# Kernel optimization log

Measured on AMD Instinct MI355X. Metric: run time of the kernel, lower is better.

The kernel has to match this reference:

```python
import jax, jax.numpy as jnp
import numpy as np

N, D, HID, ATT, B, NC = 131072, 1024, 256, 128, 64, 2
EPS = 1e-5

def _ln(h, g, b):
    mu = jnp.mean(h, axis=-1, keepdims=True)
    var = jnp.mean((h - mu) ** 2, axis=-1, keepdims=True)
    return (h - mu) * jax.lax.rsqrt(var + EPS) * g + b

def _gelu(x):
    return jax.nn.gelu(x, approximate=False)  # torch nn.GELU default (erf)

def setup_inputs() -> dict:
    key = jax.random.key(0)
    ks = jax.random.split(key, 16)
    def w(k, shape, fan_in):
        return (jax.random.normal(k, shape, jnp.float32) / np.sqrt(fan_in)).astype(jnp.float32)
    # sorted, every bag non-empty (~equal sizes)
    segment_ids = ((jnp.arange(N) * B) // N).astype(jnp.int32)
    return {
        "x": jax.random.normal(ks[0], (N, D), jnp.float32),
        "segment_ids": segment_ids,
        "W1": w(ks[1], (D, HID), D), "b1": jnp.zeros((HID,), jnp.float32),
        "g1": jnp.ones((HID,), jnp.float32), "be1": jnp.zeros((HID,), jnp.float32),
        "W2": w(ks[2], (HID, HID), HID), "b2": jnp.zeros((HID,), jnp.float32),
        "g2": jnp.ones((HID,), jnp.float32), "be2": jnp.zeros((HID,), jnp.float32),
        "Wv": w(ks[3], (HID, ATT), HID), "bv": jnp.zeros((ATT,), jnp.float32),
        "Wu": w(ks[4], (HID, ATT), HID), "bu": jnp.zeros((ATT,), jnp.float32),
        "Ww": w(ks[5], (ATT, 1), ATT), "bw": jnp.zeros((1,), jnp.float32),
        "Wc1": w(ks[6], (HID, HID // 2), HID), "bc1": jnp.zeros((HID // 2,), jnp.float32),
        "Wc2": w(ks[7], (HID // 2, NC), HID // 2), "bc2": jnp.zeros((NC,), jnp.float32),
    }

def reference(x, segment_ids, W1, b1, g1, be1, W2, b2, g2, be2,
              Wv, bv, Wu, bu, Ww, bw, Wc1, bc1, Wc2, bc2):
    # encoder (dropout = identity at inference)
    h = _gelu(_ln(x @ W1 + b1, g1, be1))          # [N, HID]
    h = _gelu(_ln(h @ W2 + b2, g2, be2))          # [N, HID]
    # gated attention logits
    a = (jnp.tanh(h @ Wv + bv) * jax.nn.sigmoid(h @ Wu + bu)) @ Ww + bw  # [N, 1]
    a = a[:, 0]                                    # [N]
    # per-bag (segment) softmax
    m = jax.ops.segment_max(a, segment_ids, num_segments=B)             # [B]
    e = jnp.exp(a - m[segment_ids])
    s = jax.ops.segment_sum(e, segment_ids, num_segments=B)             # [B]
    attn = e / s[segment_ids]                                           # [N]
    # attention-weighted bag pooling
    z = jax.ops.segment_sum(attn[:, None] * h, segment_ids, num_segments=B)  # [B, HID]
    # classifier
    logits = _gelu(z @ Wc1 + bc1) @ Wc2 + bc2       # [B, NC]
    return logits
```

## Files before the change

### kernel.cpp

```cpp
#include <hip/hip_runtime.h>
#include <math.h>

#define N_TOK  131072
#define DIM    1024
#define HIDN   256
#define ATTN   128
#define NSEG   64
#define SEGLEN 2048
#define NCLS   2
#define EPSLN  1e-5f

typedef __attribute__((ext_vector_type(8))) short  short8;
typedef __attribute__((ext_vector_type(4))) float  f32x4;

__device__ __forceinline__ unsigned short f2bf(float f) {
    unsigned int u = __float_as_uint(f);
    u += 0x7fffu + ((u >> 16) & 1u);
    return (unsigned short)(u >> 16);
}
__device__ __forceinline__ float bf2f(unsigned short h) {
    return __uint_as_float(((unsigned int)h) << 16);
}
__device__ __forceinline__ float gelu_exact(float x) {
    return 0.5f * x * (1.0f + erff(x * 0.70710678118654752f));
}

__global__ __launch_bounds__(256) void transpose_cvt(const float* __restrict__ in,
                                                     unsigned short* __restrict__ out,
                                                     int R, int C) {
    __shared__ float t[32][33];
    const int bx = blockIdx.x * 32;
    const int by = blockIdx.y * 32;
    const int x = threadIdx.x, y = threadIdx.y;
#pragma unroll
    for (int i = 0; i < 32; i += 8) {
        int r = by + y + i, c = bx + x;
        if (r < R && c < C) t[y + i][x] = in[(size_t)r * C + c];
    }
    __syncthreads();
#pragma unroll
    for (int i = 0; i < 32; i += 8) {
        int c = bx + y + i, r = by + x;
        if (c < C && r < R) out[(size_t)c * R + r] = f2bf(t[x][y + i]);
    }
}

__global__ void build_bvu(const float* __restrict__ bv, const float* __restrict__ bu,
                          float* __restrict__ bvu) {
    int t = threadIdx.x;
    bvu[t] = (t < 128) ? bv[t] : bu[t - 128];
}

template <int K, bool AF32>
__global__ __launch_bounds__(256) void gemm_bf16(const void* __restrict__ Aptr,
                                                 const unsigned short* __restrict__ Wt,
                                                 const float* __restrict__ bias,
                                                 float* __restrict__ C) {
    __shared__ unsigned short As[64][40];
    __shared__ unsigned short Ws[256][40];
    const int tid  = threadIdx.x;
    const int wave = tid >> 6, lane = tid & 63;
    const int lr = lane & 15, lq = lane >> 4;
    const int srow = tid >> 2, skq = (tid & 3) * 8;
    const size_t row0 = (size_t)blockIdx.x * 64;

    f32x4 acc[4][4];
#pragma unroll
    for (int i = 0; i < 4; i++)
#pragma unroll
        for (int j = 0; j < 4; j++) acc[i][j] = (f32x4)0.0f;

    for (int k0 = 0; k0 < K; k0 += 32) {
        short8 aw;
        if constexpr (AF32) {
            const float* A = (const float*)Aptr;
            const float* p = &A[(row0 + srow) * K + k0 + skq];
            float4 v0 = *(const float4*)p;
            float4 v1 = *(const float4*)(p + 4);
            aw[0] = (short)f2bf(v0.x); aw[1] = (short)f2bf(v0.y);
            aw[2] = (short)f2bf(v0.z); aw[3] = (short)f2bf(v0.w);
            aw[4] = (short)f2bf(v1.x); aw[5] = (short)f2bf(v1.y);
            aw[6] = (short)f2bf(v1.z); aw[7] = (short)f2bf(v1.w);
        } else {
            const unsigned short* A = (const unsigned short*)Aptr;
            aw = *(const short8*)&A[(row0 + srow) * K + k0 + skq];
        }
        short8 ww[4];
#pragma unroll
        for (int c = 0; c < 4; c++)
            ww[c] = *(const short8*)&Wt[(size_t)(srow + 64 * c) * K + k0 + skq];

        __syncthreads();
        *(short8*)&As[srow][skq] = aw;
#pragma unroll
        for (int c = 0; c < 4; c++)
            *(short8*)&Ws[srow + 64 * c][skq] = ww[c];
        __syncthreads();

        short8 a[4], b[4];
#pragma unroll
        for (int i = 0; i < 4; i++) a[i] = *(const short8*)&As[16 * i + lr][lq * 8];
#pragma unroll
        for (int j = 0; j < 4; j++) b[j] = *(const short8*)&Ws[64 * wave + 16 * j + lr][lq * 8];
#pragma unroll
        for (int i = 0; i < 4; i++)
#pragma unroll
            for (int j = 0; j < 4; j++)
                acc[i][j] = __builtin_amdgcn_mfma_f32_16x16x32_bf16(a[i], b[j], acc[i][j], 0, 0, 0);
    }

    float bj[4];
#pragma unroll
    for (int j = 0; j < 4; j++) bj[j] = bias[wave * 64 + 16 * j + lr];
#pragma unroll
    for (int i = 0; i < 4; i++)
#pragma unroll
        for (int j = 0; j < 4; j++)
#pragma unroll
            for (int r = 0; r < 4; r++)
                C[(row0 + 16 * i + lq * 4 + r) * 256 + wave * 64 + 16 * j + lr] = acc[i][j][r] + bj[j];
}

__global__ __launch_bounds__(256) void ln_gelu_cvt(const float* __restrict__ Cin,
                                                   const float* __restrict__ g,
                                                   const float* __restrict__ be,
                                                   unsigned short* __restrict__ Hout) {
    const int row  = blockIdx.x * 4 + (threadIdx.x >> 6);
    const int lane = threadIdx.x & 63;
    float4 v = *(const float4*)&Cin[(size_t)row * HIDN + lane * 4];
    float s  = v.x + v.y + v.z + v.w;
    float sq = v.x * v.x + v.y * v.y + v.z * v.z + v.w * v.w;
#pragma unroll
    for (int o = 32; o > 0; o >>= 1) { s += __shfl_down(s, o); sq += __shfl_down(sq, o); }
    s  = __shfl(s, 0);
    sq = __shfl(sq, 0);
    const float mu  = s * (1.0f / HIDN);
    const float var = sq * (1.0f / HIDN) - mu * mu;
    const float r   = rsqrtf(var + EPSLN);
    float4 gg = *(const float4*)&g[lane * 4];
    float4 bb = *(const float4*)&be[lane * 4];
    ushort4 o4;
    o4.x = f2bf(gelu_exact((v.x - mu) * r * gg.x + bb.x));
    o4.y = f2bf(gelu_exact((v.y - mu) * r * gg.y + bb.y));
    o4.z = f2bf(gelu_exact((v.z - mu) * r * gg.z + bb.z));
    o4.w = f2bf(gelu_exact((v.w - mu) * r * gg.w + bb.w));
    *(ushort4*)&Hout[(size_t)row * HIDN + lane * 4] = o4;
}

__global__ __launch_bounds__(256) void score_act(const float* __restrict__ VU,
                                                 const float* __restrict__ Ww,
                                                 const float* __restrict__ bw,
                                                 float* __restrict__ Aout) {
    const int row  = blockIdx.x * 4 + (threadIdx.x >> 6);
    const int lane = threadIdx.x & 63;
    const float* p = VU + (size_t)row * 256;
    float2 v = *(const float2*)&p[2 * lane];
    float2 u = *(const float2*)&p[128 + 2 * lane];
    float2 w = *(const float2*)&Ww[2 * lane];
    float val = tanhf(v.x) * (1.0f / (1.0f + expf(-u.x))) * w.x
              + tanhf(v.y) * (1.0f / (1.0f + expf(-u.y))) * w.y;
#pragma unroll
    for (int o = 32; o > 0; o >>= 1) val += __shfl_down(val, o);
    if (lane == 0) Aout[row] = val + bw[0];
}

__global__ __launch_bounds__(256) void seg_softmax(float* __restrict__ A) {
    __shared__ float red[256];
    const int seg = blockIdx.x, tid = threadIdx.x;
    float* a = A + (size_t)seg * SEGLEN;
    float m = -1e30f;
#pragma unroll
    for (int c = 0; c < 8; c++) m = fmaxf(m, a[tid + 256 * c]);
    red[tid] = m; __syncthreads();
    for (int s = 128; s > 0; s >>= 1) {
        if (tid < s) red[tid] = fmaxf(red[tid], red[tid + s]);
        __syncthreads();
    }
    m = red[0]; __syncthreads();
    float e[8]; float sum = 0.0f;
#pragma unroll
    for (int c = 0; c < 8; c++) { e[c] = expf(a[tid + 256 * c] - m); sum += e[c]; }
    red[tid] = sum; __syncthreads();
    for (int s = 128; s > 0; s >>= 1) {
        if (tid < s) red[tid] += red[tid + s];
        __syncthreads();
    }
    const float inv = 1.0f / red[0];
#pragma unroll
    for (int c = 0; c < 8; c++) a[tid + 256 * c] = e[c] * inv;
}

__global__ __launch_bounds__(256) void pool_partial(const float* __restrict__ Attn,
                                                    const unsigned short* __restrict__ H,
                                                    float* __restrict__ Zp) {
    __shared__ float aw[256];
    const int tid = threadIdx.x;
    const size_t rbase = (size_t)blockIdx.x * 256;
    aw[tid] = Attn[rbase + tid];
    __syncthreads();
    const unsigned short* h = H + rbase * 256 + tid;
    float acc = 0.0f;
    for (int r = 0; r < 256; r++) acc += aw[r] * bf2f(h[(size_t)r * 256]);
    Zp[rbase + tid] = acc;
}

__global__ __launch_bounds__(256) void head_kernel(const float* __restrict__ Zp,
                                                   const float* __restrict__ Wc1,
                                                   const float* __restrict__ bc1,
                                                   const float* __restrict__ Wc2,
                                                   const float* __restrict__ bc2,
                                                   float* __restrict__ Out) {
    __shared__ float zs[256];
    __shared__ float hs[128];
    __shared__ float red[4];
    const int seg = blockIdx.x, tid = threadIdx.x;
    float z = 0.0f;
#pragma unroll
    for (int c = 0; c < 8; c++) z += Zp[((size_t)seg * 8 + c) * 256 + tid];
    zs[tid] = z;
    __syncthreads();
    if (tid < 128) {
        float acc = bc1[tid];
        for (int k = 0; k < 256; k++) acc += zs[k] * Wc1[k * 128 + tid];
        hs[tid] = gelu_exact(acc);
    }
    __syncthreads();
    const int cls = tid >> 7, j = tid & 127;
    float val = hs[j] * Wc2[j * 2 + cls];
#pragma unroll
    for (int o = 32; o > 0; o >>= 1) val += __shfl_down(val, o);
    if ((tid & 63) == 0) red[tid >> 6] = val;
    __syncthreads();
    if (tid < 2) Out[seg * 2 + tid] = red[tid * 2] + red[tid * 2 + 1] + bc2[tid];
}

extern "C" void kernel_launch(void* const* d_in, const int* in_sizes, int n_in,
                              void* d_out, int out_size, void* d_ws, size_t ws_size,
                              hipStream_t stream) {
    const float* x   = (const float*)d_in[0];
    const float* W1  = (const float*)d_in[2];
    const float* b1  = (const float*)d_in[3];
    const float* g1  = (const float*)d_in[4];
    const float* be1 = (const float*)d_in[5];
    const float* W2  = (const float*)d_in[6];
    const float* b2  = (const float*)d_in[7];
    const float* g2  = (const float*)d_in[8];
    const float* be2 = (const float*)d_in[9];
    const float* Wv  = (const float*)d_in[10];
    const float* bv  = (const float*)d_in[11];
    const float* Wu  = (const float*)d_in[12];
    const float* bu  = (const float*)d_in[13];
    const float* Ww  = (const float*)d_in[14];
    const float* bw  = (const float*)d_in[15];
    const float* Wc1 = (const float*)d_in[16];
    const float* bc1 = (const float*)d_in[17];
    const float* Wc2 = (const float*)d_in[18];
    const float* bc2 = (const float*)d_in[19];
    float* out = (float*)d_out;

    char* p = (char*)d_ws;
    float*          bufA   = (float*)p;          p += (size_t)N_TOK * HIDN * 4;
    unsigned short* h1b    = (unsigned short*)p; p += (size_t)N_TOK * HIDN * 2;
    unsigned short* h2b    = (unsigned short*)p; p += (size_t)N_TOK * HIDN * 2;
    float*          scores = (float*)p;          p += (size_t)N_TOK * 4;
    unsigned short* W1t    = (unsigned short*)p; p += (size_t)HIDN * DIM * 2;
    unsigned short* W2t    = (unsigned short*)p; p += (size_t)HIDN * HIDN * 2;
    unsigned short* Wvut   = (unsigned short*)p; p += (size_t)HIDN * HIDN * 2;
    float*          bvu    = (float*)p;          p += 256 * 4;
    float*          Zp     = (float*)p;          p += (size_t)NSEG * 8 * HIDN * 4;

    dim3 tb(32, 8);
    transpose_cvt<<<dim3(HIDN / 32, DIM / 32), tb, 0, stream>>>(W1, W1t, DIM, HIDN);
    transpose_cvt<<<dim3(HIDN / 32, HIDN / 32), tb, 0, stream>>>(W2, W2t, HIDN, HIDN);
    transpose_cvt<<<dim3(ATTN / 32, HIDN / 32), tb, 0, stream>>>(Wv, Wvut, HIDN, ATTN);
    transpose_cvt<<<dim3(ATTN / 32, HIDN / 32), tb, 0, stream>>>(Wu, Wvut + (size_t)ATTN * HIDN, HIDN, ATTN);
    build_bvu<<<1, 256, 0, stream>>>(bv, bu, bvu);

    gemm_bf16<DIM, true><<<N_TOK / 64, 256, 0, stream>>>(x, W1t, b1, bufA);
    ln_gelu_cvt<<<N_TOK / 4, 256, 0, stream>>>(bufA, g1, be1, h1b);
    gemm_bf16<HIDN, false><<<N_TOK / 64, 256, 0, stream>>>(h1b, W2t, b2, bufA);
    ln_gelu_cvt<<<N_TOK / 4, 256, 0, stream>>>(bufA, g2, be2, h2b);
    gemm_bf16<HIDN, false><<<N_TOK / 64, 256, 0, stream>>>(h2b, Wvut, bvu, bufA);
    score_act<<<N_TOK / 4, 256, 0, stream>>>(bufA, Ww, bw, scores);
    seg_softmax<<<NSEG, 256, 0, stream>>>(scores);
    pool_partial<<<NSEG * 8, 256, 0, stream>>>(scores, h2b, Zp);
    head_kernel<<<NSEG, 256, 0, stream>>>(Zp, Wc1, bc1, Wc2, bc2, out);
}
```

Before: 1.025 ms.

## Fuse LayerNorm+GELU and gated-attention scoring into GEMM epilogues

Each GEMM now finishes its own epilogue in-register: the first two apply the row LayerNorm and GELU through a cross-wave reduction in shared memory and write the bf16 activations directly. The third computes tanh, sigmoid and the dot with Ww, then writes only the per-row score. This removes the fp32 intermediate buffer and three separate elementwise kernels, avoiding a write and re-read of a 128 MB fp32 tensor three times. In exchange it adds extra barriers, larger shared memory use and more register pressure in the GEMM kernels.

```diff
diff --git a/kernel.cpp b/kernel.cpp
--- a/kernel.cpp
+++ b/kernel.cpp
@@ -51,13 +51,21 @@
     bvu[t] = (t < 128) ? bv[t] : bu[t - 128];
 }
 
-template <int K, bool AF32>
-__global__ __launch_bounds__(256) void gemm_bf16(const void* __restrict__ Aptr,
-                                                 const unsigned short* __restrict__ Wt,
-                                                 const float* __restrict__ bias,
-                                                 float* __restrict__ C) {
-    __shared__ unsigned short As[64][40];
-    __shared__ unsigned short Ws[256][40];
+template <int K, int MODE, bool AF32>
+__global__ __launch_bounds__(256) void gemm_fused(const void* __restrict__ Aptr,
+                                                  const unsigned short* __restrict__ Wt,
+                                                  const float* __restrict__ bias,
+                                                  const float* __restrict__ g,
+                                                  const float* __restrict__ be,
+                                                  unsigned short* __restrict__ Hout,
+                                                  const float* __restrict__ Ww,
+                                                  const float* __restrict__ bw,
+                                                  float* __restrict__ Aout) {
+    constexpr int SMEM_BYTES = (MODE == 1) ? 33536 : 25600;
+    __shared__ __align__(16) char smem[SMEM_BYTES];
+    auto As = (unsigned short (*)[40])(smem);
+    auto Ws = (unsigned short (*)[40])(smem + 5120);
+
     const int tid  = threadIdx.x;
     const int wave = tid >> 6, lane = tid & 63;
     const int lr = lane & 15, lq = lane >> 4;
@@ -109,59 +117,94 @@
                 acc[i][j] = __builtin_amdgcn_mfma_f32_16x16x32_bf16(a[i], b[j], acc[i][j], 0, 0, 0);
     }
 
-    float bj[4];
-#pragma unroll
-    for (int j = 0; j < 4; j++) bj[j] = bias[wave * 64 + 16 * j + lr];
+    __syncthreads();
+
+    float bjv[4];
+#pragma unroll
+    for (int j = 0; j < 4; j++) bjv[j] = bias[wave * 64 + 16 * j + lr];
 #pragma unroll
     for (int i = 0; i < 4; i++)
 #pragma unroll
         for (int j = 0; j < 4; j++)
 #pragma unroll
-            for (int r = 0; r < 4; r++)
-                C[(row0 + 16 * i + lq * 4 + r) * 256 + wave * 64 + 16 * j + lr] = acc[i][j][r] + bj[j];
-}
-
-__global__ __launch_bounds__(256) void ln_gelu_cvt(const float* __restrict__ Cin,
-                                                   const float* __restrict__ g,
-                                                   const float* __restrict__ be,
-                                                   unsigned short* __restrict__ Hout) {
-    const int row  = blockIdx.x * 4 + (threadIdx.x >> 6);
-    const int lane = threadIdx.x & 63;
-    float4 v = *(const float4*)&Cin[(size_t)row * HIDN + lane * 4];
-    float s  = v.x + v.y + v.z + v.w;
-    float sq = v.x * v.x + v.y * v.y + v.z * v.z + v.w * v.w;
-#pragma unroll
-    for (int o = 32; o > 0; o >>= 1) { s += __shfl_down(s, o); sq += __shfl_down(sq, o); }
-    s  = __shfl(s, 0);
-    sq = __shfl(sq, 0);
-    const float mu  = s * (1.0f / HIDN);
-    const float var = sq * (1.0f / HIDN) - mu * mu;
-    const float r   = rsqrtf(var + EPSLN);
-    float4 gg = *(const float4*)&g[lane * 4];
-    float4 bb = *(const float4*)&be[lane * 4];
-    ushort4 o4;
-    o4.x = f2bf(gelu_exact((v.x - mu) * r * gg.x + bb.x));
-    o4.y = f2bf(gelu_exact((v.y - mu) * r * gg.y + bb.y));
-    o4.z = f2bf(gelu_exact((v.z - mu) * r * gg.z + bb.z));
-    o4.w = f2bf(gelu_exact((v.w - mu) * r * gg.w + bb.w));
-    *(ushort4*)&Hout[(size_t)row * HIDN + lane * 4] = o4;
-}
-
-__global__ __launch_bounds__(256) void score_act(const float* __restrict__ VU,
-                                                 const float* __restrict__ Ww,
-                                                 const float* __restrict__ bw,
-                                                 float* __restrict__ Aout) {
-    const int row  = blockIdx.x * 4 + (threadIdx.x >> 6);
-    const int lane = threadIdx.x & 63;
-    const float* p = VU + (size_t)row * 256;
-    float2 v = *(const float2*)&p[2 * lane];
-    float2 u = *(const float2*)&p[128 + 2 * lane];
-    float2 w = *(const float2*)&Ww[2 * lane];
-    float val = tanhf(v.x) * (1.0f / (1.0f + expf(-u.x))) * w.x
-              + tanhf(v.y) * (1.0f / (1.0f + expf(-u.y))) * w.y;
-#pragma unroll
-    for (int o = 32; o > 0; o >>= 1) val += __shfl_down(val, o);
-    if (lane == 0) Aout[row] = val + bw[0];
+            for (int r = 0; r < 4; r++) acc[i][j][r] += bjv[j];
+
+    if constexpr (MODE == 0) {
+        float (*red)[4][64] = (float (*)[4][64])smem;
+#pragma unroll
+        for (int i = 0; i < 4; i++)
+#pragma unroll
+            for (int r = 0; r < 4; r++) {
+                float s = 0.0f, sq = 0.0f;
+#pragma unroll
+                for (int j = 0; j < 4; j++) { float v = acc[i][j][r]; s += v; sq += v * v; }
+#pragma unroll
+                for (int m = 1; m < 16; m <<= 1) { s += __shfl_xor(s, m); sq += __shfl_xor(sq, m); }
+                if (lr == 0) {
+                    red[0][wave][16 * i + 4 * lq + r] = s;
+                    red[1][wave][16 * i + 4 * lq + r] = sq;
+                }
+            }
+        __syncthreads();
+        float gj[4], bej[4];
+#pragma unroll
+        for (int j = 0; j < 4; j++) {
+            gj[j]  = g[wave * 64 + 16 * j + lr];
+            bej[j] = be[wave * 64 + 16 * j + lr];
+        }
+#pragma unroll
+        for (int i = 0; i < 4; i++)
+#pragma unroll
+            for (int r = 0; r < 4; r++) {
+                const int row = 16 * i + 4 * lq + r;
+                const float s  = red[0][0][row] + red[0][1][row] + red[0][2][row] + red[0][3][row];
+                const float sq = red[1][0][row] + red[1][1][row] + red[1][2][row] + red[1][3][row];
+                const float mu  = s * (1.0f / HIDN);
+                const float var = sq * (1.0f / HIDN) - mu * mu;
+                const float rs  = rsqrtf(var + EPSLN);
+#pragma unroll
+                for (int j = 0; j < 4; j++) {
+                    const float o = (acc[i][j][r] - mu) * rs * gj[j] + bej[j];
+                    Hout[(row0 + row) * 256 + wave * 64 + 16 * j + lr] = f2bf(gelu_exact(o));
+                }
+            }
+    } else {
+        float (*us)[129] = (float (*)[129])smem;
+        float (*pw)[64]  = (float (*)[64])(smem + 33024);
+        if (wave >= 2) {
+            const int cb = (wave - 2) * 64;
+#pragma unroll
+            for (int i = 0; i < 4; i++)
+#pragma unroll
+                for (int j = 0; j < 4; j++)
+#pragma unroll
+                    for (int r = 0; r < 4; r++)
+                        us[16 * i + 4 * lq + r][cb + 16 * j + lr] =
+                            1.0f / (1.0f + expf(-acc[i][j][r]));
+        }
+        __syncthreads();
+        if (wave < 2) {
+            const int cb = wave * 64;
+            float wwj[4];
+#pragma unroll
+            for (int j = 0; j < 4; j++) wwj[j] = Ww[cb + 16 * j + lr];
+#pragma unroll
+            for (int i = 0; i < 4; i++)
+#pragma unroll
+                for (int r = 0; r < 4; r++) {
+                    const int row = 16 * i + 4 * lq + r;
+                    float s = 0.0f;
+#pragma unroll
+                    for (int j = 0; j < 4; j++)
+                        s += tanhf(acc[i][j][r]) * us[row][cb + 16 * j + lr] * wwj[j];
+#pragma unroll
+                    for (int m = 1; m < 16; m <<= 1) s += __shfl_xor(s, m);
+                    if (lr == 0) pw[wave][row] = s;
+                }
+        }
+        __syncthreads();
+        if (tid < 64) Aout[row0 + tid] = pw[0][tid] + pw[1][tid] + bw[0];
+    }
 }
 
 __global__ __launch_bounds__(256) void seg_softmax(float* __restrict__ A) {
@@ -259,7 +302,6 @@
     float* out = (float*)d_out;
 
     char* p = (char*)d_ws;
-    float*          bufA   = (float*)p;          p += (size_t)N_TOK * HIDN * 4;
     unsigned short* h1b    = (unsigned short*)p; p += (size_t)N_TOK * HIDN * 2;
     unsigned short* h2b    = (unsigned short*)p; p += (size_t)N_TOK * HIDN * 2;
     float*          scores = (float*)p;          p += (size_t)N_TOK * 4;
@@ -276,12 +318,13 @@
     transpose_cvt<<<dim3(ATTN / 32, HIDN / 32), tb, 0, stream>>>(Wu, Wvut + (size_t)ATTN * HIDN, HIDN, ATTN);
     build_bvu<<<1, 256, 0, stream>>>(bv, bu, bvu);
 
-    gemm_bf16<DIM, true><<<N_TOK / 64, 256, 0, stream>>>(x, W1t, b1, bufA);
-    ln_gelu_cvt<<<N_TOK / 4, 256, 0, stream>>>(bufA, g1, be1, h1b);
-    gemm_bf16<HIDN, false><<<N_TOK / 64, 256, 0, stream>>>(h1b, W2t, b2, bufA);
-    ln_gelu_cvt<<<N_TOK / 4, 256, 0, stream>>>(bufA, g2, be2, h2b);
-    gemm_bf16<HIDN, false><<<N_TOK / 64, 256, 0, stream>>>(h2b, Wvut, bvu, bufA);
-    score_act<<<N_TOK / 4, 256, 0, stream>>>(bufA, Ww, bw, scores);
+    gemm_fused<DIM, 0, true><<<N_TOK / 64, 256, 0, stream>>>(
+        x, W1t, b1, g1, be1, h1b, nullptr, nullptr, nullptr);
+    gemm_fused<HIDN, 0, false><<<N_TOK / 64, 256, 0, stream>>>(
+        h1b, W2t, b2, g2, be2, h2b, nullptr, nullptr, nullptr);
+    gemm_fused<HIDN, 1, false><<<N_TOK / 64, 256, 0, stream>>>(
+        h2b, Wvut, bvu, nullptr, nullptr, nullptr, Ww, bw, scores);
+
     seg_softmax<<<NSEG, 256, 0, stream>>>(scores);
     pool_partial<<<NSEG * 8, 256, 0, stream>>>(scores, h2b, Zp);
     head_kernel<<<NSEG, 256, 0, stream>>>(Zp, Wc1, bc1, Wc2, bc2, out);
```

New measurement: 1.008 ms. About the same (-1.7%).
